# Kernel optimization log

Measured on AMD Instinct MI355X. Metric: run time of the kernel, lower is better.

Reference implementation:

```python
import jax, jax.numpy as jnp
import numpy as np

N_NODES = 100000
N_EDGES = 800000
HIDDEN = 64
N_LAYERS = 3
N_TYPES = 64
LN_EPS = 1e-5


def setup_inputs() -> dict:
    key = jax.random.key(0)
    ks = jax.random.split(key, 10)
    type_indices = jax.random.randint(ks[0], (N_NODES,), 0, N_TYPES)
    edges = jax.random.randint(ks[1], (N_EDGES, 2), 0, N_NODES)
    s = 1.0 / np.sqrt(2 * HIDDEN)
    return {
        "type_indices": type_indices,
        "edges": edges,
        "embed_table": jax.random.normal(ks[2], (N_TYPES, HIDDEN), jnp.float32),
        "msg_w": jax.random.uniform(ks[3], (N_LAYERS, 2 * HIDDEN, HIDDEN), jnp.float32, -s, s),
        "msg_b": jax.random.uniform(ks[4], (N_LAYERS, HIDDEN), jnp.float32, -s, s),
        "upd_w": jax.random.uniform(ks[5], (N_LAYERS, 2 * HIDDEN, HIDDEN), jnp.float32, -s, s),
        "upd_b": jax.random.uniform(ks[6], (N_LAYERS, HIDDEN), jnp.float32, -s, s),
        "ln_g": jnp.ones((N_LAYERS, HIDDEN), jnp.float32),
        "ln_b": jnp.zeros((N_LAYERS, HIDDEN), jnp.float32),
    }


def _layer_norm(h, g, b):
    mu = h.mean(-1, keepdims=True)
    var = ((h - mu) ** 2).mean(-1, keepdims=True)
    return (h - mu) * jax.lax.rsqrt(var + LN_EPS) * g + b


def reference(type_indices, edges, embed_table, msg_w, msg_b, upd_w, upd_b, ln_g, ln_b):
    N = type_indices.shape[0]
    src, tgt = edges[:, 0], edges[:, 1]
    x = embed_table[type_indices]                          # [N, D]
    for i in range(N_LAYERS):
        # per-edge: gather src/tgt features, linear + relu message
        m_in = jnp.concatenate([x[src], x[tgt]], axis=-1)  # [E, 2D]
        msg = jax.nn.relu(m_in @ msg_w[i] + msg_b[i])      # [E, D]
        # scatter-mean by target node
        agg = jax.ops.segment_sum(msg, tgt, num_segments=N)
        cnt = jax.ops.segment_sum(jnp.ones_like(tgt, dtype=x.dtype), tgt, num_segments=N)
        agg = agg / jnp.clip(cnt, 1.0)[:, None]
        # residual update + LayerNorm
        u = jax.nn.relu(jnp.concatenate([x, agg], axis=-1) @ upd_w[i] + upd_b[i])
        x = _layer_norm(u + x, ln_g[i], ln_b[i])
    # global readout: mean + max pooling
    return jnp.concatenate([x.mean(axis=0), x.max(axis=0)])
```

## Files before the change

kernel.cpp:

```cpp
#include <hip/hip_runtime.h>
#include <hip/hip_fp16.h>
#include <math.h>

#define NND 100000
#define NED 800000
#define NLAY 3
#define BSH 9
#define NBKT ((NND + 511) / 512)
#define CAP 8192
#define GB  ((NND + 63) / 64)
static constexpr float LNEPS = 1e-5f;

typedef __attribute__((ext_vector_type(8))) short short8;
typedef __attribute__((ext_vector_type(4))) float floatx4;
typedef __attribute__((ext_vector_type(2))) float floatx2;

__device__ __forceinline__ short f2bf(float f) {
    unsigned u = __float_as_uint(f);
    u += 0x7fffu + ((u >> 16) & 1u);
    return (short)(u >> 16);
}
__device__ __forceinline__ float bf2f(short s) {
    return __uint_as_float(((unsigned)(unsigned short)s) << 16);
}

__device__ __forceinline__ void load_h8(const __half* p, float* f) {
    uint4 v = *(const uint4*)p;
    unsigned a[4] = {v.x, v.y, v.z, v.w};
#pragma unroll
    for (int k = 0; k < 4; k++) {
        __half2 h = *(__half2*)&a[k];
        float2 g = __half22float2(h);
        f[2 * k] = g.x; f[2 * k + 1] = g.y;
    }
}

__device__ __forceinline__ void unpack_f8x16(uint4 v, float* f) {
    unsigned a[4] = {v.x, v.y, v.z, v.w};
#pragma unroll
    for (int k = 0; k < 4; k++) {
        floatx2 lo = __builtin_amdgcn_cvt_pk_f32_fp8(a[k], false);
        floatx2 hi = __builtin_amdgcn_cvt_pk_f32_fp8(a[k], true);
        f[4 * k + 0] = lo[0]; f[4 * k + 1] = lo[1];
        f[4 * k + 2] = hi[0]; f[4 * k + 3] = hi[1];
    }
}
__device__ __forceinline__ unsigned char f32_to_fp8(float v) {
    int r = __builtin_amdgcn_cvt_pk_fp8_f32(v, v, 0, false);
    return (unsigned char)(r & 0xff);
}

__global__ void k_init(int* __restrict__ gtail) {
    int gt = blockIdx.x * blockDim.x + threadIdx.x;
    if (gt < NBKT) gtail[gt] = gt * CAP;
}

__global__ __launch_bounds__(256) void k_bscatter(const int2* __restrict__ e, int* __restrict__ gtail,
                                                  long long* __restrict__ tmp) {
    __shared__ int cnt[NBKT], chunk[NBKT], cur[NBKT];
    const int T = 2048;
    int ntile = (NED + T - 1) / T;
    for (int tile = blockIdx.x; tile < ntile; tile += gridDim.x) {
        int base = tile * T;
        int t = threadIdx.x;
        for (int i = t; i < NBKT; i += 256) { cnt[i] = 0; cur[i] = 0; }
        __syncthreads();
        int2 ed[8]; int bk[8];
#pragma unroll
        for (int i = 0; i < 8; i++) {
            int idx = base + i * 256 + t;
            if (idx < NED) {
                ed[i] = e[idx];
                bk[i] = ((unsigned)ed[i].y) >> BSH;
                atomicAdd(&cnt[bk[i]], 1);
            } else bk[i] = -1;
        }
        __syncthreads();
        for (int i = t; i < NBKT; i += 256) if (cnt[i]) chunk[i] = atomicAdd(&gtail[i], cnt[i]);
        __syncthreads();
#pragma unroll
        for (int i = 0; i < 8; i++) {
            if (bk[i] >= 0) {
                int r = atomicAdd(&cur[bk[i]], 1);
                tmp[(size_t)chunk[bk[i]] + r] =
                    ((long long)(unsigned)ed[i].y << 32) | (unsigned)ed[i].x;
            }
        }
        __syncthreads();
    }
}

__global__ __launch_bounds__(512) void k_bfinish(const long long* __restrict__ tmp, const int* __restrict__ gtail,
                                                 int* __restrict__ rowb, int* __restrict__ degv,
                                                 int* __restrict__ srcs) {
    __shared__ int ld[512];
    __shared__ int lcur[512];
    int b = blockIdx.x, t = threadIdx.x;
    int node0 = b << BSH;
    int nn = min(512, NND - node0);
    int ebase = b * CAP, eend = gtail[b];
    ld[t] = 0;
    __syncthreads();
    for (int i = ebase + t; i < eend; i += 512) {
        int tgt = (int)(tmp[i] >> 32);
        atomicAdd(&ld[tgt - node0], 1);
    }
    __syncthreads();
    int v = ld[t];
    for (int off = 1; off < 512; off <<= 1) {
        int u = (t >= off) ? ld[t - off] : 0;
        __syncthreads();
        ld[t] += u;
        __syncthreads();
    }
    int exc = ld[t] - v;
    if (t < nn) { rowb[node0 + t] = ebase + exc; degv[node0 + t] = v; }
    lcur[t] = exc;
    __syncthreads();
    for (int i = ebase + t; i < eend; i += 512) {
        long long pk = tmp[i];
        int tgt = (int)(pk >> 32);
        int src = (int)(pk & 0xffffffffll);
        int p = atomicAdd(&lcur[tgt - node0], 1);
        srcs[ebase + p] = src;
    }
}

__global__ void k_prep(const float* __restrict__ msg_w, const float* __restrict__ upd_w,
                       short* __restrict__ wmsg, short* __restrict__ wupd) {
    int t = blockIdx.x * blockDim.x + threadIdx.x;
    if (t >= 2 * NLAY * 8192) return;
    int which = t / (NLAY * 8192);
    int e = t % (NLAY * 8192);
    int l = e >> 13, idx = e & 8191;
    int j = idx & 7, lane = (idx >> 3) & 63, hi = idx >> 9;
    int lm = lane & 15, quad = lane >> 4;
    if (which == 0) {
        int ks = hi & 1, nt = hi >> 1;
        int n = nt * 16 + lm, k = ks * 32 + quad * 8 + j;
        float v = (n < 64) ? msg_w[(size_t)l * 8192 + k * 64 + n]
                           : msg_w[(size_t)l * 8192 + (64 + k) * 64 + (n - 64)];
        wmsg[e] = f2bf(v);
    } else {
        int ks = hi & 3, nt = hi >> 2;
        int n = nt * 16 + lm, k = ks * 32 + quad * 8 + j;
        wupd[e] = f2bf(upd_w[(size_t)l * 8192 + k * 64 + n]);
    }
}

__global__ __launch_bounds__(256) void k_pq(const int* __restrict__ ty, const float* __restrict__ tab,
                                            const short* __restrict__ wb, const float* __restrict__ bg,
                                            unsigned char* __restrict__ P8, __half* __restrict__ Q16,
                                            short* __restrict__ x16) {
    __shared__ unsigned char outs[64 * 272];
    int wv = threadIdx.x >> 6, lane = threadIdx.x & 63;
    int lm = lane & 15, quad = lane >> 4;
    int nbase = blockIdx.x * 64;
    int m = nbase + wv * 16 + lm;
    short8 a[2];
    if (m < NND) {
        const float* tr = tab + ty[m] * 64;
#pragma unroll
        for (int ks = 0; ks < 2; ks++) {
            float4 v0 = *(const float4*)(tr + ks * 32 + quad * 8);
            float4 v1 = *(const float4*)(tr + ks * 32 + quad * 8 + 4);
            short8 av;
            av[0] = f2bf(v0.x); av[1] = f2bf(v0.y); av[2] = f2bf(v0.z); av[3] = f2bf(v0.w);
            av[4] = f2bf(v1.x); av[5] = f2bf(v1.y); av[6] = f2bf(v1.z); av[7] = f2bf(v1.w);
            a[ks] = av;
            *(short8*)(x16 + (size_t)m * 64 + ks * 32 + quad * 8) = av;
        }
    } else {
#pragma unroll
        for (int ks = 0; ks < 2; ks++) { short8 z; for (int j = 0; j < 8; j++) z[j] = 0; a[ks] = z; }
    }
    floatx4 acc[8];
#pragma unroll
    for (int nt = 0; nt < 8; nt++) acc[nt] = (floatx4){0.f, 0.f, 0.f, 0.f};
#pragma unroll
    for (int nt = 0; nt < 8; nt++) {
        short8 b0 = *(const short8*)(wb + (size_t)((nt * 2 + 0) * 64 + lane) * 8);
        short8 b1 = *(const short8*)(wb + (size_t)((nt * 2 + 1) * 64 + lane) * 8);
        acc[nt] = __builtin_amdgcn_mfma_f32_16x16x32_bf16(a[0], b0, acc[nt], 0, 0, 0);
        acc[nt] = __builtin_amdgcn_mfma_f32_16x16x32_bf16(a[1], b1, acc[nt], 0, 0, 0);
    }
    float bq[4];
#pragma unroll
    for (int nt = 0; nt < 4; nt++) bq[nt] = bg[nt * 16 + lm];
#pragma unroll
    for (int reg = 0; reg < 4; reg++) {
        int rown = wv * 16 + quad * 4 + reg;
        unsigned char* rb = outs + rown * 272;
#pragma unroll
        for (int nt = 0; nt < 4; nt++)
            rb[nt * 16 + lm] = f32_to_fp8(acc[nt][reg]);
#pragma unroll
        for (int nt = 4; nt < 8; nt++)
            *(__half*)(rb + 64 + (((nt - 4) * 16 + lm) << 1)) = __float2half(acc[nt][reg] + bq[nt - 4]);
    }
#pragma unroll
    for (int pass = 0; pass < 3; pass++) {
        int idx = pass * 64 + lane;
        int ndl = (idx * 171) >> 11;
        int seg = idx - ndl * 12;
        int rown = wv * 16 + ndl;
        int gn = nbase + rown;
        if (gn < NND) {
            int off = (seg < 4) ? seg * 16 : 64 + (seg - 4) * 16;
            uint4 v = *(const uint4*)(outs + rown * 272 + off);
            if (seg < 4) *(uint4*)(P8 + (size_t)gn * 64 + seg * 16) = v;
            else *(uint4*)((char*)Q16 + (size_t)gn * 128 + (seg - 4) * 16) = v;
        }
    }
}

__global__ __launch_bounds__(256, 4) void k_aggupd(short* __restrict__ x16, const unsigned char* __restrict__ P8,
                                                   const __half* __restrict__ Q16,
                                                   const int* __restrict__ rowb, const int* __restrict__ degv,
                                                   const int* __restrict__ srcs,
                                                   const short* __restrict__ wu, const float* __restrict__ ub,
                                                   const float* __restrict__ lg, const float* __restrict__ lb,
                                                   const short* __restrict__ wm, const float* __restrict__ bgn,
                                                   unsigned char* __restrict__ Pout, __half* __restrict__ Qout,
                                                   float* __restrict__ pscratch, int last) {
    __shared__ float aggs[64 * 68];
    __shared__ float redsum[64];
    __shared__ unsigned redmax[64];
    int t = threadIdx.x, w = t >> 6, lane = t & 63;

    if (last) {
        if (t < 64) redsum[t] = 0.f;
        else if (t < 128) redmax[t - 64] = 0u;
        __syncthreads();
    }

    {
        int ln = lane >> 2, fq = lane & 3, c0 = fq * 16;
        int bn = w * 16 + ln;
        int wid = blockIdx.x * 64 + bn;
        float acc[16];
#pragma unroll
        for (int k = 0; k < 16; k++) acc[k] = 0.f;
        if (wid < NND) {
            int beg = rowb[wid], dg = degv[wid], end = beg + dg;
            float qv[16];
            load_h8(Q16 + (size_t)wid * 64 + c0, qv);
            load_h8(Q16 + (size_t)wid * 64 + c0 + 8, qv + 8);
            for (int e = beg; e < end; e += 8) {
                int last_e = end - 1;
                int s[8];
#pragma unroll
                for (int i = 0; i < 8; i++) {
                    int ei = e + i;
                    s[i] = srcs[ei < end ? ei : last_e];
                }
                uint4 pk[8];
#pragma unroll
                for (int i = 0; i < 8; i++)
                    pk[i] = *(const uint4*)(P8 + (size_t)s[i] * 64 + c0);
#pragma unroll
                for (int i = 0; i < 8; i++) {
                    if (e + i < end) {
                        float f[16];
                        unpack_f8x16(pk[i], f);
#pragma unroll
                        for (int k = 0; k < 16; k++) acc[k] += fmaxf(f[k] + qv[k], 0.f);
                    }
                }
            }
            float inv = 1.f / fmaxf((float)dg, 1.f);
#pragma unroll
            for (int s4 = 0; s4 < 4; s4++)
                *(float4*)(aggs + bn * 68 + c0 + s4 * 4) =
                    make_float4(acc[s4 * 4] * inv, acc[s4 * 4 + 1] * inv,
                                acc[s4 * 4 + 2] * inv, acc[s4 * 4 + 3] * inv);
        } else {
#pragma unroll
            for (int s4 = 0; s4 < 4; s4++)
                *(float4*)(aggs + bn * 68 + c0 + s4 * 4) = make_float4(0.f, 0.f, 0.f, 0.f);
        }
    }

    int lm = lane & 15, quad = lane >> 4;
    int m = blockIdx.x * 64 + w * 16 + lm;
    int bm = w * 16 + lm;

    short8 a[4];
#pragma unroll
    for (int ks = 0; ks < 2; ks++) {
        if (m < NND) a[ks] = *(const short8*)(x16 + (size_t)m * 64 + ks * 32 + quad * 8);
        else { short8 z; for (int j = 0; j < 8; j++) z[j] = 0; a[ks] = z; }
    }
#pragma unroll
    for (int ks = 2; ks < 4; ks++) {
        const float* p = aggs + bm * 68 + (ks - 2) * 32 + quad * 8;
        float4 v0 = *(const float4*)p;
        float4 v1 = *(const float4*)(p + 4);
        float xv[8] = {v0.x, v0.y, v0.z, v0.w, v1.x, v1.y, v1.z, v1.w};
        short8 av;
#pragma unroll
        for (int j = 0; j < 8; j++) av[j] = f2bf(xv[j]);
        a[ks] = av;
    }
    floatx4 acc4[4];
#pragma unroll
    for (int nt = 0; nt < 4; nt++) acc4[nt] = (floatx4){0.f, 0.f, 0.f, 0.f};
#pragma unroll
    for (int nt = 0; nt < 4; nt++) {
#pragma unroll
        for (int ks = 0; ks < 4; ks++) {
            short8 b = *(const short8*)(wu + (size_t)((nt * 4 + ks) * 64 + lane) * 8);
            acc4[nt] = __builtin_amdgcn_mfma_f32_16x16x32_bf16(a[ks], b, acc4[nt], 0, 0, 0);
        }
    }
    float ubv[4], lgv[4], lbv[4];
#pragma unroll
    for (int nt = 0; nt < 4; nt++) {
        int col = nt * 16 + lm;
        ubv[nt] = ub[col]; lgv[nt] = lg[col]; lbv[nt] = lb[col];
    }
    float csum[4] = {0.f, 0.f, 0.f, 0.f};
    float cmax[4] = {-3.402823466e38f, -3.402823466e38f, -3.402823466e38f, -3.402823466e38f};
#pragma unroll
    for (int reg = 0; reg < 4; reg++) {
        int rown = w * 16 + quad * 4 + reg;
        int gn = blockIdx.x * 64 + rown;
        bool ok = gn < NND;
        float h[4];
#pragma unroll
        for (int nt = 0; nt < 4; nt++) {
            float xv = ok ? bf2f(x16[(size_t)gn * 64 + nt * 16 + lm]) : 0.f;
            float u = fmaxf(acc4[nt][reg] + ubv[nt], 0.f);
            h[nt] = u + xv;
        }
        float s1 = h[0] + h[1] + h[2] + h[3];
        float s2 = h[0] * h[0] + h[1] * h[1] + h[2] * h[2] + h[3] * h[3];
#pragma unroll
        for (int off = 1; off < 16; off *= 2) {
            s1 += __shfl_xor(s1, off);
            s2 += __shfl_xor(s2, off);
        }
        float mu = s1 * (1.f / 64.f);
        float var = s2 * (1.f / 64.f) - mu * mu;
        float rs = rsqrtf(var + LNEPS);
#pragma unroll
        for (int nt = 0; nt < 4; nt++) {
            float res = (h[nt] - mu) * rs * lgv[nt] + lbv[nt];
            if (!last) {
                if (ok) x16[(size_t)gn * 64 + nt * 16 + lm] = f2bf(res);
                aggs[rown * 68 + nt * 16 + lm] = res;
            } else if (ok) {
                csum[nt] += res;
                cmax[nt] = fmaxf(cmax[nt], res);
            }
        }
    }

    if (last) {
#pragma unroll
        for (int nt = 0; nt < 4; nt++) {
            csum[nt] += __shfl_xor(csum[nt], 16);
            csum[nt] += __shfl_xor(csum[nt], 32);
            cmax[nt] = fmaxf(cmax[nt], __shfl_xor(cmax[nt], 16));
            cmax[nt] = fmaxf(cmax[nt], __shfl_xor(cmax[nt], 32));
        }
        if (quad == 0) {
#pragma unroll
            for (int nt = 0; nt < 4; nt++) {
                atomicAdd(&redsum[nt * 16 + lm], csum[nt]);
                unsigned b = __float_as_uint(cmax[nt]);
                unsigned enc = (b & 0x80000000u) ? ~b : (b | 0x80000000u);
                atomicMax(&redmax[nt * 16 + lm], enc);
            }
        }
        __syncthreads();
        float* ps = pscratch + (size_t)blockIdx.x * 128;
        if (t < 64) {
            ps[t] = redsum[t];
        } else if (t < 128) {
            unsigned u = redmax[t - 64];
            unsigned b = (u & 0x80000000u) ? (u & 0x7fffffffu) : ~u;
            ps[t] = __uint_as_float(b);
        }
        return;
    }

    {
        unsigned char* bs = (unsigned char*)aggs;
        short8 na[2];
#pragma unroll
        for (int ks = 0; ks < 2; ks++) {
            const float* p = aggs + bm * 68 + ks * 32 + quad * 8;
            float4 v0 = *(const float4*)p;
            float4 v1 = *(const float4*)(p + 4);
            float xv[8] = {v0.x, v0.y, v0.z, v0.w, v1.x, v1.y, v1.z, v1.w};
            short8 av;
#pragma unroll
            for (int j = 0; j < 8; j++) av[j] = f2bf(xv[j]);
            na[ks] = av;
        }
        floatx4 c8[8];
#pragma unroll
        for (int nt = 0; nt < 8; nt++) c8[nt] = (floatx4){0.f, 0.f, 0.f, 0.f};
#pragma unroll
        for (int nt = 0; nt < 8; nt++) {
            short8 b0 = *(const short8*)(wm + (size_t)((nt * 2 + 0) * 64 + lane) * 8);
            short8 b1 = *(const short8*)(wm + (size_t)((nt * 2 + 1) * 64 + lane) * 8);
            c8[nt] = __builtin_amdgcn_mfma_f32_16x16x32_bf16(na[0], b0, c8[nt], 0, 0, 0);
            c8[nt] = __builtin_amdgcn_mfma_f32_16x16x32_bf16(na[1], b1, c8[nt], 0, 0, 0);
        }
        float bq[4];
#pragma unroll
        for (int nt = 0; nt < 4; nt++) bq[nt] = bgn[nt * 16 + lm];
#pragma unroll
        for (int reg = 0; reg < 4; reg++) {
            int rown = w * 16 + quad * 4 + reg;
            unsigned char* rb = bs + rown * 272;
#pragma unroll
            for (int nt = 0; nt < 4; nt++)
                rb[nt * 16 + lm] = f32_to_fp8(c8[nt][reg]);
#pragma unroll
            for (int nt = 4; nt < 8; nt++)
                *(__half*)(rb + 64 + (((nt - 4) * 16 + lm) << 1)) = __float2half(c8[nt][reg] + bq[nt - 4]);
        }
#pragma unroll
        for (int pass = 0; pass < 3; pass++) {
            int idx = pass * 64 + lane;
            int ndl = (idx * 171) >> 11;
            int seg = idx - ndl * 12;
            int rown = w * 16 + ndl;
            int gn = blockIdx.x * 64 + rown;
            if (gn < NND) {
                int off = (seg < 4) ? seg * 16 : 64 + (seg - 4) * 16;
                uint4 v = *(const uint4*)(bs + rown * 272 + off);
                if (seg < 4) *(uint4*)(Pout + (size_t)gn * 64 + seg * 16) = v;
                else *(uint4*)((char*)Qout + (size_t)gn * 128 + (seg - 4) * 16) = v;
            }
        }
    }
}

__global__ __launch_bounds__(256) void k_fin(const float* __restrict__ pscratch, float* __restrict__ out) {
    __shared__ float sm[256];
    int b = blockIdx.x;
    int t = threadIdx.x;
    bool issum = b < 64;
    float v = issum ? 0.f : -3.402823466e38f;
    for (int i = t; i < GB; i += 256) {
        float x = pscratch[(size_t)i * 128 + b];
        v = issum ? (v + x) : fmaxf(v, x);
    }
    sm[t] = v; __syncthreads();
    for (int off = 128; off > 0; off >>= 1) {
        if (t < off) sm[t] = issum ? (sm[t] + sm[t + off]) : fmaxf(sm[t], sm[t + off]);
        __syncthreads();
    }
    if (t == 0) out[b] = issum ? sm[0] * (1.f / (float)NND) : sm[0];
}

extern "C" void kernel_launch(void* const* d_in, const int* in_sizes, int n_in,
                              void* d_out, int out_size, void* d_ws, size_t ws_size,
                              hipStream_t stream) {
    const int* ty      = (const int*)d_in[0];
    const int* ed      = (const int*)d_in[1];
    const float* tab   = (const float*)d_in[2];
    const float* msg_w = (const float*)d_in[3];
    const float* msg_b = (const float*)d_in[4];
    const float* upd_w = (const float*)d_in[5];
    const float* upd_b = (const float*)d_in[6];
    const float* ln_g  = (const float*)d_in[7];
    const float* ln_b  = (const float*)d_in[8];
    float* out = (float*)d_out;

    char* w = (char*)d_ws;
    auto alloc = [&](size_t sz) { char* p = w; w += (sz + 255) & ~(size_t)255; return p; };
    short* x16         = (short*)alloc((size_t)NND * 64 * 2);
    unsigned char* P0  = (unsigned char*)alloc((size_t)NND * 64);
    unsigned char* P1  = (unsigned char*)alloc((size_t)NND * 64);
    __half* Q0         = (__half*)alloc((size_t)NND * 64 * 2);
    __half* Q1         = (__half*)alloc((size_t)NND * 64 * 2);
    long long* tmp     = (long long*)alloc((size_t)NBKT * CAP * 8);
    int* srcs          = (int*)alloc((size_t)NBKT * CAP * 4);
    int* rowb          = (int*)alloc((size_t)NND * 4);
    int* degv          = (int*)alloc((size_t)NND * 4);
    int* gtail         = (int*)alloc(256 * 4);
    float* pscratch    = (float*)alloc((size_t)GB * 128 * 4);
    short* wmsg        = (short*)alloc((size_t)NLAY * 8192 * 2);
    short* wupd        = (short*)alloc((size_t)NLAY * 8192 * 2);

    k_init<<<1, 256, 0, stream>>>(gtail);
    k_prep<<<(2 * NLAY * 8192 + 255) / 256, 256, 0, stream>>>(msg_w, upd_w, wmsg, wupd);
    k_bscatter<<<(NED + 2047) / 2048, 256, 0, stream>>>((const int2*)ed, gtail, tmp);
    k_bfinish<<<NBKT, 512, 0, stream>>>(tmp, gtail, rowb, degv, srcs);

    k_pq<<<GB, 256, 0, stream>>>(ty, tab, wmsg, msg_b, P0, Q0, x16);

    k_aggupd<<<GB, 256, 0, stream>>>(x16, P0, Q0, rowb, degv, srcs,
                                     wupd + 0 * 8192, upd_b + 0, ln_g + 0, ln_b + 0,
                                     wmsg + 1 * 8192, msg_b + 64, P1, Q1, pscratch, 0);
    k_aggupd<<<GB, 256, 0, stream>>>(x16, P1, Q1, rowb, degv, srcs,
                                     wupd + 1 * 8192, upd_b + 64, ln_g + 64, ln_b + 64,
                                     wmsg + 2 * 8192, msg_b + 128, P0, Q0, pscratch, 0);
    k_aggupd<<<GB, 256, 0, stream>>>(x16, P0, Q0, rowb, degv, srcs,
                                     wupd + 2 * 8192, upd_b + 128, ln_g + 128, ln_b + 128,
                                     wmsg + 2 * 8192, msg_b + 128, P1, Q1, pscratch, 1);

    k_fin<<<128, 256, 0, stream>>>(pscratch, out);
}
```

Before: 221.1 us.

## Split aggregation across eight lanes per node with 512-thread blocks

```diff
diff --git a/kernel.cpp b/kernel.cpp
--- a/kernel.cpp
+++ b/kernel.cpp
@@ -35,10 +35,10 @@
     }
 }
 
-__device__ __forceinline__ void unpack_f8x16(uint4 v, float* f) {
-    unsigned a[4] = {v.x, v.y, v.z, v.w};
-#pragma unroll
-    for (int k = 0; k < 4; k++) {
+__device__ __forceinline__ void unpack_f8x8(uint2 v, float* f) {
+    unsigned a[2] = {v.x, v.y};
+#pragma unroll
+    for (int k = 0; k < 2; k++) {
         floatx2 lo = __builtin_amdgcn_cvt_pk_f32_fp8(a[k], false);
         floatx2 hi = __builtin_amdgcn_cvt_pk_f32_fp8(a[k], true);
         f[4 * k + 0] = lo[0]; f[4 * k + 1] = lo[1];
@@ -214,7 +214,7 @@
     }
 }
 
-__global__ __launch_bounds__(256, 4) void k_aggupd(short* __restrict__ x16, const unsigned char* __restrict__ P8,
+__global__ __launch_bounds__(512, 4) void k_aggupd(short* __restrict__ x16, const unsigned char* __restrict__ P8,
                                                    const __half* __restrict__ Q16,
                                                    const int* __restrict__ rowb, const int* __restrict__ degv,
                                                    const int* __restrict__ srcs,
@@ -223,10 +223,11 @@
                                                    const short* __restrict__ wm, const float* __restrict__ bgn,
                                                    unsigned char* __restrict__ Pout, __half* __restrict__ Qout,
                                                    float* __restrict__ pscratch, int last) {
-    __shared__ float aggs[64 * 68];
+    __shared__ float aggs[128 * 68];
     __shared__ float redsum[64];
     __shared__ unsigned redmax[64];
     int t = threadIdx.x, w = t >> 6, lane = t & 63;
+    int gw = blockIdx.x * 64 + w * 8;
 
     if (last) {
         if (t < 64) redsum[t] = 0.f;
@@ -235,17 +236,16 @@
     }
 
     {
-        int ln = lane >> 2, fq = lane & 3, c0 = fq * 16;
+        int ln = lane >> 3, f8 = lane & 7, c0 = f8 * 8;
         int bn = w * 16 + ln;
-        int wid = blockIdx.x * 64 + bn;
-        float acc[16];
-#pragma unroll
-        for (int k = 0; k < 16; k++) acc[k] = 0.f;
+        int wid = gw + ln;
+        float acc[8];
+#pragma unroll
+        for (int k = 0; k < 8; k++) acc[k] = 0.f;
         if (wid < NND) {
             int beg = rowb[wid], dg = degv[wid], end = beg + dg;
-            float qv[16];
+            float qv[8];
             load_h8(Q16 + (size_t)wid * 64 + c0, qv);
-            load_h8(Q16 + (size_t)wid * 64 + c0 + 8, qv + 8);
             for (int e = beg; e < end; e += 8) {
                 int last_e = end - 1;
                 int s[8];
@@ -254,41 +254,40 @@
                     int ei = e + i;
                     s[i] = srcs[ei < end ? ei : last_e];
                 }
-                uint4 pk[8];
+                uint2 pk[8];
 #pragma unroll
                 for (int i = 0; i < 8; i++)
-                    pk[i] = *(const uint4*)(P8 + (size_t)s[i] * 64 + c0);
+                    pk[i] = *(const uint2*)(P8 + (size_t)s[i] * 64 + c0);
 #pragma unroll
                 for (int i = 0; i < 8; i++) {
                     if (e + i < end) {
-                        float f[16];
-                        unpack_f8x16(pk[i], f);
-#pragma unroll
-                        for (int k = 0; k < 16; k++) acc[k] += fmaxf(f[k] + qv[k], 0.f);
+                        float f[8];
+                        unpack_f8x8(pk[i], f);
+#pragma unroll
+                        for (int k = 0; k < 8; k++) acc[k] += fmaxf(f[k] + qv[k], 0.f);
                     }
                 }
             }
             float inv = 1.f / fmaxf((float)dg, 1.f);
-#pragma unroll
-            for (int s4 = 0; s4 < 4; s4++)
-                *(float4*)(aggs + bn * 68 + c0 + s4 * 4) =
-                    make_float4(acc[s4 * 4] * inv, acc[s4 * 4 + 1] * inv,
-                                acc[s4 * 4 + 2] * inv, acc[s4 * 4 + 3] * inv);
+            *(float4*)(aggs + bn * 68 + c0)     = make_float4(acc[0] * inv, acc[1] * inv, acc[2] * inv, acc[3] * inv);
+            *(float4*)(aggs + bn * 68 + c0 + 4) = make_float4(acc[4] * inv, acc[5] * inv, acc[6] * inv, acc[7] * inv);
         } else {
-#pragma unroll
-            for (int s4 = 0; s4 < 4; s4++)
-                *(float4*)(aggs + bn * 68 + c0 + s4 * 4) = make_float4(0.f, 0.f, 0.f, 0.f);
-        }
+            *(float4*)(aggs + bn * 68 + c0)     = make_float4(0.f, 0.f, 0.f, 0.f);
+            *(float4*)(aggs + bn * 68 + c0 + 4) = make_float4(0.f, 0.f, 0.f, 0.f);
+        }
+        int zr = w * 16 + 8 + ln;
+        *(float4*)(aggs + zr * 68 + c0)     = make_float4(0.f, 0.f, 0.f, 0.f);
+        *(float4*)(aggs + zr * 68 + c0 + 4) = make_float4(0.f, 0.f, 0.f, 0.f);
     }
 
     int lm = lane & 15, quad = lane >> 4;
-    int m = blockIdx.x * 64 + w * 16 + lm;
+    int m = gw + lm;
     int bm = w * 16 + lm;
 
     short8 a[4];
 #pragma unroll
     for (int ks = 0; ks < 2; ks++) {
-        if (m < NND) a[ks] = *(const short8*)(x16 + (size_t)m * 64 + ks * 32 + quad * 8);
+        if (lm < 8 && m < NND) a[ks] = *(const short8*)(x16 + (size_t)m * 64 + ks * 32 + quad * 8);
         else { short8 z; for (int j = 0; j < 8; j++) z[j] = 0; a[ks] = z; }
     }
 #pragma unroll
@@ -323,9 +322,10 @@
     float cmax[4] = {-3.402823466e38f, -3.402823466e38f, -3.402823466e38f, -3.402823466e38f};
 #pragma unroll
     for (int reg = 0; reg < 4; reg++) {
-        int rown = w * 16 + quad * 4 + reg;
-        int gn = blockIdx.x * 64 + rown;
-        bool ok = gn < NND;
+        int rt = quad * 4 + reg;
+        bool valid = rt < 8;
+        int gn = gw + rt;
+        bool ok = valid && gn < NND;
         float h[4];
 #pragma unroll
         for (int nt = 0; nt < 4; nt++) {
@@ -347,8 +347,10 @@
         for (int nt = 0; nt < 4; nt++) {
             float res = (h[nt] - mu) * rs * lgv[nt] + lbv[nt];
             if (!last) {
-                if (ok) x16[(size_t)gn * 64 + nt * 16 + lm] = f2bf(res);
-                aggs[rown * 68 + nt * 16 + lm] = res;
+                if (ok) {
+                    x16[(size_t)gn * 64 + nt * 16 + lm] = f2bf(res);
+                    aggs[(w * 16 + rt) * 68 + nt * 16 + lm] = res;
+                }
             } else if (ok) {
                 csum[nt] += res;
                 cmax[nt] = fmaxf(cmax[nt], res);
@@ -414,7 +416,8 @@
         for (int nt = 0; nt < 4; nt++) bq[nt] = bgn[nt * 16 + lm];
 #pragma unroll
         for (int reg = 0; reg < 4; reg++) {
-            int rown = w * 16 + quad * 4 + reg;
+            int rt = quad * 4 + reg;
+            int rown = w * 16 + rt;
             unsigned char* rb = bs + rown * 272;
 #pragma unroll
             for (int nt = 0; nt < 4; nt++)
@@ -424,17 +427,18 @@
                 *(__half*)(rb + 64 + (((nt - 4) * 16 + lm) << 1)) = __float2half(c8[nt][reg] + bq[nt - 4]);
         }
 #pragma unroll
-        for (int pass = 0; pass < 3; pass++) {
+        for (int pass = 0; pass < 2; pass++) {
             int idx = pass * 64 + lane;
-            int ndl = (idx * 171) >> 11;
-            int seg = idx - ndl * 12;
-            int rown = w * 16 + ndl;
-            int gn = blockIdx.x * 64 + rown;
-            if (gn < NND) {
-                int off = (seg < 4) ? seg * 16 : 64 + (seg - 4) * 16;
-                uint4 v = *(const uint4*)(bs + rown * 272 + off);
-                if (seg < 4) *(uint4*)(Pout + (size_t)gn * 64 + seg * 16) = v;
-                else *(uint4*)((char*)Qout + (size_t)gn * 128 + (seg - 4) * 16) = v;
+            if (idx < 96) {
+                int ndl = idx / 12, seg = idx - ndl * 12;
+                int rown = w * 16 + ndl;
+                int gn = gw + ndl;
+                if (gn < NND) {
+                    int off = (seg < 4) ? seg * 16 : 64 + (seg - 4) * 16;
+                    uint4 v = *(const uint4*)(bs + rown * 272 + off);
+                    if (seg < 4) *(uint4*)(Pout + (size_t)gn * 64 + seg * 16) = v;
+                    else *(uint4*)((char*)Qout + (size_t)gn * 128 + (seg - 4) * 16) = v;
+                }
             }
         }
     }
@@ -495,13 +499,13 @@
 
     k_pq<<<GB, 256, 0, stream>>>(ty, tab, wmsg, msg_b, P0, Q0, x16);
 
-    k_aggupd<<<GB, 256, 0, stream>>>(x16, P0, Q0, rowb, degv, srcs,
+    k_aggupd<<<GB, 512, 0, stream>>>(x16, P0, Q0, rowb, degv, srcs,
                                      wupd + 0 * 8192, upd_b + 0, ln_g + 0, ln_b + 0,
                                      wmsg + 1 * 8192, msg_b + 64, P1, Q1, pscratch, 0);
-    k_aggupd<<<GB, 256, 0, stream>>>(x16, P1, Q1, rowb, degv, srcs,
+    k_aggupd<<<GB, 512, 0, stream>>>(x16, P1, Q1, rowb, degv, srcs,
                                      wupd + 1 * 8192, upd_b + 64, ln_g + 64, ln_b + 64,
                                      wmsg + 2 * 8192, msg_b + 128, P0, Q0, pscratch, 0);
-    k_aggupd<<<GB, 256, 0, stream>>>(x16, P0, Q0, rowb, degv, srcs,
+    k_aggupd<<<GB, 512, 0, stream>>>(x16, P0, Q0, rowb, degv, srcs,
                                      wupd + 2 * 8192, upd_b + 128, ln_g + 128, ln_b + 128,
                                      wmsg + 2 * 8192, msg_b + 128, P1, Q1, pscratch, 1);
 
```

After: 251.8 us. +13.9%, slower.
